# Kernel optimization log

Measured on AMD Instinct MI355X. Metric: run time of the kernel, lower is better.

The kernel has to match this reference:

```python
import jax, jax.numpy as jnp
import numpy as np

C = 256   # descriptor_dim
H = 4     # num_heads
D = C // H  # head_dim = 64
B, N = 8, 2048


def _conv1x1(x, w, b):
    # 1x1 Conv1d == per-position linear over channels: x [B,C,N], w [O,C], b [O]
    return jnp.einsum('oc,bcn->bon', w, x) + b[None, :, None]


def setup_inputs() -> dict:
    key = jax.random.key(0)
    ks = jax.random.split(key, 11)
    s = 1.0 / np.sqrt(C)
    return {
        'query': jax.random.normal(ks[0], (B, C, N), dtype=jnp.float32),
        'key':   jax.random.normal(ks[1], (B, C, N), dtype=jnp.float32),
        'value': jax.random.normal(ks[2], (B, C, N), dtype=jnp.float32),
        'wq': jax.random.normal(ks[3], (C, C), dtype=jnp.float32) * s,
        'bq': jax.random.normal(ks[4], (C,), dtype=jnp.float32) * s,
        'wk': jax.random.normal(ks[5], (C, C), dtype=jnp.float32) * s,
        'bk': jax.random.normal(ks[6], (C,), dtype=jnp.float32) * s,
        'wv': jax.random.normal(ks[7], (C, C), dtype=jnp.float32) * s,
        'bv': jax.random.normal(ks[8], (C,), dtype=jnp.float32) * s,
        'wm': jax.random.normal(ks[9], (C, C), dtype=jnp.float32) * s,
        'bm': jax.random.normal(ks[10], (C,), dtype=jnp.float32) * s,
    }


def reference(query, key, value, wq, bq, wk, bk, wv, bv, wm, bm):
    b = query.shape[0]
    # project then view channels as (head_dim, num_heads) -- matches torch .view order
    q = _conv1x1(query, wq, bq).reshape(b, D, H, -1)   # [B,D,H,N]
    k = _conv1x1(key,   wk, bk).reshape(b, D, H, -1)   # [B,D,H,M]
    v = _conv1x1(value, wv, bv).reshape(b, D, H, -1)   # [B,D,H,M]
    scores = jnp.einsum('bdhn,bdhm->bhnm', q, k) / (D ** 0.5)
    probs = jax.nn.softmax(scores, axis=-1)            # [B,H,N,M]
    out = jnp.einsum('bhnm,bdhm->bdhn', probs, v)      # [B,D,H,N]
    out = out.reshape(b, D * H, -1)                    # [B,C,N]
    return _conv1x1(out, wm, bm)
```

## Files before the change

kernel.cpp:

```cpp
#include <hip/hip_runtime.h>
#include <hip/hip_bf16.h>

typedef float f32x4 __attribute__((ext_vector_type(4)));
typedef float f32x16 __attribute__((ext_vector_type(16)));
typedef __bf16 bf16x8 __attribute__((ext_vector_type(8)));
typedef __bf16 bf16x4 __attribute__((ext_vector_type(4)));
typedef unsigned int uint2v __attribute__((ext_vector_type(2)));
typedef unsigned int u32;

constexpr int B_ = 8, C_ = 256, N_ = 2048, H_ = 4, D_ = 64;
constexpr int BH_ = B_ * H_;
constexpr size_t PER_ = (size_t)BH_ * N_ * D_;
constexpr float LOG2E = 1.44269504088896340736f;

static __device__ __forceinline__ float fast_exp2(float x) {
#if __has_builtin(__builtin_amdgcn_exp2f)
  return __builtin_amdgcn_exp2f(x);
#else
  return exp2f(x);
#endif
}

static __device__ __forceinline__ void* swz(void* base, int row, int cb) {
  return (char*)base + row * 128 + (cb ^ ((row & 7) << 4));
}
static __device__ __forceinline__ const void* swz(const void* base, int row, int cb) {
  return (const char*)base + row * 128 + (cb ^ ((row & 7) << 4));
}

static __device__ __forceinline__ void gload16(void* lds, const void* g) {
  __builtin_amdgcn_global_load_lds(
      (const __attribute__((address_space(1))) u32*)g,
      (__attribute__((address_space(3))) u32*)lds, 16, 0, 0);
}

struct W4 {
  const float* s0; const float* s1; const float* s2; const float* s3;
  __bf16* d0; __bf16* d1; __bf16* d2; __bf16* d3;
};

__global__ __launch_bounds__(256) void wcvt_kernel(W4 p) {
  const int m = blockIdx.y;
  const float* src = m == 0 ? p.s0 : m == 1 ? p.s1 : m == 2 ? p.s2 : p.s3;
  __bf16* dst = m == 0 ? p.d0 : m == 1 ? p.d1 : m == 2 ? p.d2 : p.d3;
  const int f = blockIdx.x * 256 + threadIdx.x;
  const int o_blk = f >> 9;
  const int ks = (f >> 6) & 7;
  const int lane = f & 63;
  const int row = o_blk * 16 + (lane & 15);
  const int kbase = ks * 32 + (lane >> 4) * 8;
  bf16x8 v;
  if (m == 3) {
    for (int e = 0; e < 8; e++) {
      const int k = kbase + e;
      const int c = ((k & 63) << 2) | (k >> 6);
      v[e] = (__bf16)src[row * 256 + c];
    }
  } else {
    const int srow = ((row & 63) << 2) | (row >> 6);
    const float* s = src + srow * 256 + kbase;
    float4 a = *(const float4*)s;
    float4 b = *(const float4*)(s + 4);
    v[0] = (__bf16)a.x; v[1] = (__bf16)a.y; v[2] = (__bf16)a.z; v[3] = (__bf16)a.w;
    v[4] = (__bf16)b.x; v[5] = (__bf16)b.y; v[6] = (__bf16)b.z; v[7] = (__bf16)b.w;
  }
  *(bf16x8*)&dst[(size_t)f * 8] = v;
}

__global__ __launch_bounds__(256) void qkv_fused_kernel(
    const float* __restrict__ xq, const float* __restrict__ xk,
    const float* __restrict__ xv, const __bf16* __restrict__ wfq,
    const __bf16* __restrict__ wfk, const __bf16* __restrict__ wfv,
    const float* __restrict__ bq, const float* __restrict__ bk,
    const float* __restrict__ bv, __bf16* __restrict__ oq,
    char* __restrict__ oksw, char* __restrict__ ovsw) {
  __shared__ __bf16 xlds[64][264];

  const int m = blockIdx.x >> 8;
  int inner = blockIdx.x & 255;
  inner = (inner & 7) * 32 + (inner >> 3);
  const int b = inner >> 5, nb = inner & 31;
  const int n0 = nb * 64;

  const float* xf = m == 0 ? xq : m == 1 ? xk : xv;
  const __bf16* wf = m == 0 ? wfq : m == 1 ? wfk : wfv;
  const float* bias = m == 0 ? bq : m == 1 ? bk : bv;
  const float scale = m == 0 ? 0.125f * LOG2E : 1.0f;

  const int t = threadIdx.x;
  {
    const int kl = t & 15;
    const int nl = (t >> 4) * 4;
    const float* src = xf + (size_t)b * C_ * N_ + n0 + nl;
    for (int kp = 0; kp < 8; kp++) {
      const int k = kp * 32 + kl * 2;
      float4 f0 = *(const float4*)(src + (size_t)k * N_);
      float4 f1 = *(const float4*)(src + (size_t)(k + 1) * N_);
      union { __bf16 h[2]; u32 u; } c0, c1, c2, c3;
      c0.h[0] = (__bf16)f0.x; c0.h[1] = (__bf16)f1.x;
      c1.h[0] = (__bf16)f0.y; c1.h[1] = (__bf16)f1.y;
      c2.h[0] = (__bf16)f0.z; c2.h[1] = (__bf16)f1.z;
      c3.h[0] = (__bf16)f0.w; c3.h[1] = (__bf16)f1.w;
      *(u32*)&xlds[nl + 0][k] = c0.u;
      *(u32*)&xlds[nl + 1][k] = c1.u;
      *(u32*)&xlds[nl + 2][k] = c2.u;
      *(u32*)&xlds[nl + 3][k] = c3.u;
    }
  }
  __syncthreads();

  const int lane = t & 63, wvv = t >> 6;
  const int wm = wvv >> 1, wn = wvv & 1;
  const int l15 = lane & 15, lg = lane >> 4;

  f32x4 acc[8][2] = {};

  for (int ks = 0; ks < 8; ks++) {
    bf16x8 bfr[2];
    for (int ni = 0; ni < 2; ni++)
      bfr[ni] = *(const bf16x8*)&xlds[wn * 32 + ni * 16 + l15][ks * 32 + lg * 8];
    for (int mi = 0; mi < 8; mi++) {
      bf16x8 af = *(const bf16x8*)&wf[(((size_t)(wm * 8 + mi) * 8 + ks) * 64 + lane) * 8];
      acc[mi][0] = __builtin_amdgcn_mfma_f32_16x16x32_bf16(af, bfr[0], acc[mi][0], 0, 0, 0);
      acc[mi][1] = __builtin_amdgcn_mfma_f32_16x16x32_bf16(af, bfr[1], acc[mi][1], 0, 0, 0);
    }
  }

  for (int mi = 0; mi < 8; mi++) {
    const int h = wm * 2 + (mi >> 2);
    const int d0 = (mi & 3) * 16 + 4 * lg;
    for (int ni = 0; ni < 2; ni++) {
      const int n = n0 + wn * 32 + ni * 16 + l15;
      const size_t tbase = ((size_t)(b * H_ + h) * (N_ / 64) + (n >> 6)) * 8192;
      if (m == 0) {
        bf16x4 o4;
        for (int r = 0; r < 4; r++)
          o4[r] = (__bf16)((acc[mi][ni][r] + bias[((d0 + r) << 2) | h]) * scale);
        *(bf16x4*)&oq[((size_t)(b * H_ + h) * N_ + n) * D_ + d0] = o4;
      } else if (m == 1) {
        bf16x4 o4;
        for (int r = 0; r < 4; r++)
          o4[r] = (__bf16)(acc[mi][ni][r] + bias[((d0 + r) << 2) | h]);
        *(bf16x4*)swz(oksw + tbase, n & 63, 2 * d0) = o4;
      } else {
        for (int r = 0; r < 4; r++)
          *(__bf16*)swz(ovsw + tbase, d0 + r, 2 * (n & 63)) =
              (__bf16)(acc[mi][ni][r] + bias[((d0 + r) << 2) | h]);
      }
    }
  }
}

template <int COMB>
__global__ __launch_bounds__(256) void final_proj_kernel(
    const __bf16* __restrict__ p0, const __bf16* __restrict__ p1,
    const float* __restrict__ l0, const float* __restrict__ l1,
    const __bf16* __restrict__ wf, const float* __restrict__ bias,
    float* __restrict__ out) {
  const int bid = blockIdx.x;
  const int wid = (bid & 7) * 128 + (bid >> 3);
  const int o_t = wid & 3;
  const int nb = (wid >> 2) & 31;
  const int b = wid >> 7;
  const int o0 = o_t * 64, n0 = nb * 64;
  const int t = threadIdx.x, lane = t & 63;
  const int wvv = t >> 6, wm = wvv >> 1, wn = wvv & 1;
  const int l15 = lane & 15, lg = lane >> 4;
  const int nbase = n0 + wn * 32 + l15;

  float inv[2][4];
  if constexpr (COMB) {
    for (int ni = 0; ni < 2; ni++)
      for (int h = 0; h < 4; h++) {
        const size_t bhn = (size_t)(b * H_ + h) * N_ + nbase + ni * 16;
        inv[ni][h] = 1.f / (l0[bhn] + l1[bhn]);
      }
  }

  f32x4 acc[2][2] = {};

  for (int ks = 0; ks < 8; ks++) {
    bf16x8 af[2];
    for (int mi = 0; mi < 2; mi++)
      af[mi] = *(const bf16x8*)&wf[(((size_t)(o_t * 4 + wm * 2 + mi) * 8 + ks) * 64 + lane) * 8];
    bf16x8 bfr[2];
    const int h = ks >> 1;
    const size_t bh = (size_t)(b * H_ + h);
    const int d0 = (ks & 1) * 32 + lg * 8;
    for (int ni = 0; ni < 2; ni++) {
      const size_t off = (bh * N_ + nbase + ni * 16) * D_ + d0;
      bf16x8 a = *(const bf16x8*)&p0[off];
      if constexpr (COMB) {
        bf16x8 bb = *(const bf16x8*)&p1[off];
        const float iv = inv[ni][h];
        bf16x8 r;
#pragma unroll
        for (int e = 0; e < 8; e++)
          r[e] = (__bf16)(((float)a[e] + (float)bb[e]) * iv);
        bfr[ni] = r;
      } else {
        bfr[ni] = a;
      }
    }
    for (int mi = 0; mi < 2; mi++)
      for (int ni = 0; ni < 2; ni++)
        acc[mi][ni] = __builtin_amdgcn_mfma_f32_16x16x32_bf16(
            af[mi], bfr[ni], acc[mi][ni], 0, 0, 0);
  }

  for (int mi = 0; mi < 2; mi++) {
    for (int r = 0; r < 4; r++) {
      const int och = o0 + wm * 32 + mi * 16 + 4 * lg + r;
      const float bv_ = bias[och];
      for (int ni = 0; ni < 2; ni++) {
        const int n = n0 + wn * 32 + ni * 16 + l15;
        out[((size_t)b * C_ + och) * N_ + n] = acc[mi][ni][r] + bv_;
      }
    }
  }
}

template <int SPLIT>
__global__ __launch_bounds__(256) void attn_kernel(
    const __bf16* __restrict__ qb, const char* __restrict__ kbsw,
    const char* __restrict__ vtsw, __bf16* __restrict__ pO,
    float* __restrict__ lbuf) {
  __shared__ char smem[32768];

  const int t = threadIdx.x, lane = t & 63, wv = t >> 6;
  const int l31 = lane & 31, hi = lane >> 5;

  const int bid = blockIdx.x;
  const int per_xcd = (512 * SPLIT) / 8;
  const int wid = (bid & 7) * per_xcd + (bid >> 3);
  const int bh = wid / (16 * SPLIT);
  const int rem = wid % (16 * SPLIT);
  const int qt = rem & 15;
  const int s = rem >> 4;
  const int qn = qt * 128 + wv * 32;
  constexpr int NT = N_ / SPLIT / 64;
  const int jt0 = s * NT;

  const char* ktiles = kbsw + (size_t)bh * (N_ / 64) * 8192;
  const char* vtiles = vtsw + (size_t)bh * (N_ / 64) * 8192;

  const __bf16* qrow = qb + ((size_t)bh * N_ + qn + l31) * D_;
  bf16x8 qf[4];
#pragma unroll
  for (int i = 0; i < 4; i++) qf[i] = *(const bf16x8*)(qrow + i * 16 + hi * 8);

  auto stage = [&](int jt_g, int bb) {
    const char* kt = ktiles + (size_t)jt_g * 8192;
    const char* vt = vtiles + (size_t)jt_g * 8192;
    gload16(smem + bb * 8192 + t * 16, kt + t * 16);
    gload16(smem + bb * 8192 + 4096 + t * 16, kt + 4096 + t * 16);
    gload16(smem + 16384 + bb * 8192 + t * 16, vt + t * 16);
    gload16(smem + 16384 + bb * 8192 + 4096 + t * 16, vt + 4096 + t * 16);
  };

  stage(jt0, 0);
  __syncthreads();

  f32x16 o0 = {}, o1 = {};
  float la0 = 0.f, la1 = 0.f, la2 = 0.f, la3 = 0.f;
  int cur = 0;

  for (int jt = 0; jt < NT; jt++) {
    if (jt + 1 < NT) stage(jt0 + jt + 1, cur ^ 1);
    const char* kc = smem + cur * 8192;
    const char* vc = smem + 16384 + cur * 8192;

    f32x16 s0 = {}, s1 = {};
    __builtin_amdgcn_s_setprio(1);
#pragma unroll
    for (int i = 0; i < 4; i++) {
      bf16x8 kf = *(const bf16x8*)swz(kc, l31, i * 32 + hi * 16);
      s0 = __builtin_amdgcn_mfma_f32_32x32x16_bf16(kf, qf[i], s0, 0, 0, 0);
    }
#pragma unroll
    for (int i = 0; i < 4; i++) {
      bf16x8 kf = *(const bf16x8*)swz(kc, 32 + l31, i * 32 + hi * 16);
      s1 = __builtin_amdgcn_mfma_f32_32x32x16_bf16(kf, qf[i], s1, 0, 0, 0);
    }
    __builtin_amdgcn_s_setprio(0);

#pragma unroll
    for (int sub = 0; sub < 2; sub++) {
      const f32x16 sv = sub ? s1 : s0;
      float pr[16];
#pragma unroll
      for (int r = 0; r < 16; r++) pr[r] = fast_exp2(sv[r]);
      la0 += pr[0] + pr[4] + pr[8] + pr[12];
      la1 += pr[1] + pr[5] + pr[9] + pr[13];
      la2 += pr[2] + pr[6] + pr[10] + pr[14];
      la3 += pr[3] + pr[7] + pr[11] + pr[15];
      unsigned w[8];
#pragma unroll
      for (int g = 0; g < 8; g++) {
        union { __bf16 h[2]; unsigned u; } cv;
        cv.h[0] = (__bf16)pr[2 * g];
        cv.h[1] = (__bf16)pr[2 * g + 1];
        w[g] = cv.u;
      }
      uint2v r0 = __builtin_amdgcn_permlane32_swap(w[0], w[2], false, false);
      uint2v r1 = __builtin_amdgcn_permlane32_swap(w[1], w[3], false, false);
      uint2v r2 = __builtin_amdgcn_permlane32_swap(w[4], w[6], false, false);
      uint2v r3 = __builtin_amdgcn_permlane32_swap(w[5], w[7], false, false);
      union { unsigned u[4]; bf16x8 v; } f0 = {{r0.x, r1.x, r0.y, r1.y}};
      union { unsigned u[4]; bf16x8 v; } f1 = {{r2.x, r3.x, r2.y, r3.y}};
      const int scb = sub * 64;
      __builtin_amdgcn_s_setprio(1);
      {
        bf16x8 vf = *(const bf16x8*)swz(vc, l31, scb + hi * 16);
        o0 = __builtin_amdgcn_mfma_f32_32x32x16_bf16(vf, f0.v, o0, 0, 0, 0);
        vf = *(const bf16x8*)swz(vc, l31, scb + 32 + hi * 16);
        o0 = __builtin_amdgcn_mfma_f32_32x32x16_bf16(vf, f1.v, o0, 0, 0, 0);
        vf = *(const bf16x8*)swz(vc, 32 + l31, scb + hi * 16);
        o1 = __builtin_amdgcn_mfma_f32_32x32x16_bf16(vf, f0.v, o1, 0, 0, 0);
        vf = *(const bf16x8*)swz(vc, 32 + l31, scb + 32 + hi * 16);
        o1 = __builtin_amdgcn_mfma_f32_32x32x16_bf16(vf, f1.v, o1, 0, 0, 0);
      }
      __builtin_amdgcn_s_setprio(0);
    }

    __syncthreads();
    cur ^= 1;
  }

  float la = la0 + la1 + la2 + la3;
  la += __shfl_xor(la, 32);
  const float scl = (SPLIT == 1) ? 1.f / la : 1.f;

  if constexpr (SPLIT > 1) {
    if (hi == 0)
      lbuf[(size_t)s * BH_ * N_ + (size_t)bh * N_ + qn + l31] = la;
  }

  char* ep = smem + wv * 4096;
#pragma unroll
  for (int dt = 0; dt < 2; dt++) {
    const f32x16 o = dt ? o1 : o0;
#pragma unroll
    for (int g = 0; g < 4; g++) {
      bf16x4 o4;
#pragma unroll
      for (int j = 0; j < 4; j++) o4[j] = (__bf16)(o[4 * g + j] * scl);
      *(bf16x4*)swz(ep, l31, dt * 64 + 16 * g + 8 * hi) = o4;
    }
  }
  asm volatile("" ::: "memory");
  {
    __bf16* dst = pO + (size_t)s * PER_ + ((size_t)bh * N_ + qn) * D_;
#pragma unroll
    for (int i = 0; i < 4; i++) {
      const int row = i * 8 + (lane >> 3);
      uint4 v = *(const uint4*)swz(ep, row, (lane & 7) * 16);
      *(uint4*)((char*)dst + i * 1024 + lane * 16) = v;
    }
  }
}

extern "C" void kernel_launch(void* const* d_in, const int* in_sizes, int n_in,
                              void* d_out, int out_size, void* d_ws,
                              size_t ws_size, hipStream_t stream) {
  const float* query = (const float*)d_in[0];
  const float* key_ = (const float*)d_in[1];
  const float* value = (const float*)d_in[2];
  const float* wq = (const float*)d_in[3];
  const float* bq = (const float*)d_in[4];
  const float* wk = (const float*)d_in[5];
  const float* bk = (const float*)d_in[6];
  const float* wv = (const float*)d_in[7];
  const float* bv = (const float*)d_in[8];
  const float* wm = (const float*)d_in[9];
  const float* bm = (const float*)d_in[10];

  __bf16* qb = (__bf16*)d_ws;
  char* kbsw = (char*)(qb + PER_);
  char* vtsw = kbsw + PER_ * 2;
  __bf16* p0 = (__bf16*)(vtsw + PER_ * 2);
  __bf16* p1 = p0 + PER_;
  float* lbuf = (float*)(p1 + PER_);
  __bf16* wfq = (__bf16*)(lbuf + 2 * BH_ * N_);
  __bf16* wfk = wfq + 65536;
  __bf16* wfv = wfk + 65536;
  __bf16* wfm = wfv + 65536;

  const size_t need_split = (size_t)((char*)(wfm + 65536) - (char*)d_ws);
  const bool use_split = ws_size >= need_split;

  dim3 blk(256);
  W4 wp{wq, wk, wv, wm, wfq, wfk, wfv, wfm};
  if (!use_split) {
    wfq = p1; wfk = wfq + 65536; wfv = wfk + 65536; wfm = wfv + 65536;
    wp = W4{wq, wk, wv, wm, wfq, wfk, wfv, wfm};
  }
  wcvt_kernel<<<dim3(32, 4), blk, 0, stream>>>(wp);

  qkv_fused_kernel<<<768, blk, 0, stream>>>(query, key_, value, wfq, wfk, wfv,
                                            bq, bk, bv, qb, kbsw, vtsw);
  if (use_split) {
    attn_kernel<2><<<1024, blk, 0, stream>>>(qb, kbsw, vtsw, p0, lbuf);
    final_proj_kernel<1><<<1024, blk, 0, stream>>>(
        p0, p1, lbuf, lbuf + BH_ * N_, wfm, bm, (float*)d_out);
  } else {
    attn_kernel<1><<<512, blk, 0, stream>>>(qb, kbsw, vtsw, p0, nullptr);
    final_proj_kernel<0><<<1024, blk, 0, stream>>>(
        p0, p0, nullptr, nullptr, wfm, bm, (float*)d_out);
  }
}
```

Before: 106.5 us.

## Use 512-thread attention blocks with 4-way KV split and generalized combine

The attention kernel now runs 8 waves per block, covering 256 query rows that share each staged K/V tile, so each thread loads half as much per tile. The key dimension is split up to 4 ways when workspace allows, which restores the block count. The final projection is generalized to sum NS partial outputs and NS row-sum buffers before normalizing. This raises K/V reuse per block and keeps parallelism, but the combine step reads more partial data and needs more workspace. The workspace layout is reordered to fit the extra partials.

```diff
diff --git a/kernel.cpp b/kernel.cpp
--- a/kernel.cpp
+++ b/kernel.cpp
@@ -151,10 +151,9 @@
   }
 }
 
-template <int COMB>
+template <int NS>
 __global__ __launch_bounds__(256) void final_proj_kernel(
-    const __bf16* __restrict__ p0, const __bf16* __restrict__ p1,
-    const float* __restrict__ l0, const float* __restrict__ l1,
+    const __bf16* __restrict__ p, const float* __restrict__ lb,
     const __bf16* __restrict__ wf, const float* __restrict__ bias,
     float* __restrict__ out) {
   const int bid = blockIdx.x;
@@ -169,11 +168,14 @@
   const int nbase = n0 + wn * 32 + l15;
 
   float inv[2][4];
-  if constexpr (COMB) {
+  if constexpr (NS > 1) {
     for (int ni = 0; ni < 2; ni++)
       for (int h = 0; h < 4; h++) {
         const size_t bhn = (size_t)(b * H_ + h) * N_ + nbase + ni * 16;
-        inv[ni][h] = 1.f / (l0[bhn] + l1[bhn]);
+        float ls = 0.f;
+#pragma unroll
+        for (int u = 0; u < NS; u++) ls += lb[(size_t)u * BH_ * N_ + bhn];
+        inv[ni][h] = 1.f / ls;
       }
   }
 
@@ -189,17 +191,21 @@
     const int d0 = (ks & 1) * 32 + lg * 8;
     for (int ni = 0; ni < 2; ni++) {
       const size_t off = (bh * N_ + nbase + ni * 16) * D_ + d0;
-      bf16x8 a = *(const bf16x8*)&p0[off];
-      if constexpr (COMB) {
-        bf16x8 bb = *(const bf16x8*)&p1[off];
+      if constexpr (NS == 1) {
+        bfr[ni] = *(const bf16x8*)&p[off];
+      } else {
+        float s8[8] = {};
+#pragma unroll
+        for (int u = 0; u < NS; u++) {
+          bf16x8 a = *(const bf16x8*)&p[(size_t)u * PER_ + off];
+#pragma unroll
+          for (int e = 0; e < 8; e++) s8[e] += (float)a[e];
+        }
         const float iv = inv[ni][h];
         bf16x8 r;
 #pragma unroll
-        for (int e = 0; e < 8; e++)
-          r[e] = (__bf16)(((float)a[e] + (float)bb[e]) * iv);
+        for (int e = 0; e < 8; e++) r[e] = (__bf16)(s8[e] * iv);
         bfr[ni] = r;
-      } else {
-        bfr[ni] = a;
       }
     }
     for (int mi = 0; mi < 2; mi++)
@@ -221,7 +227,7 @@
 }
 
 template <int SPLIT>
-__global__ __launch_bounds__(256) void attn_kernel(
+__global__ __launch_bounds__(512) void attn_kernel(
     const __bf16* __restrict__ qb, const char* __restrict__ kbsw,
     const char* __restrict__ vtsw, __bf16* __restrict__ pO,
     float* __restrict__ lbuf) {
@@ -231,13 +237,13 @@
   const int l31 = lane & 31, hi = lane >> 5;
 
   const int bid = blockIdx.x;
-  const int per_xcd = (512 * SPLIT) / 8;
+  const int per_xcd = (256 * SPLIT) / 8;
   const int wid = (bid & 7) * per_xcd + (bid >> 3);
-  const int bh = wid / (16 * SPLIT);
-  const int rem = wid % (16 * SPLIT);
-  const int qt = rem & 15;
-  const int s = rem >> 4;
-  const int qn = qt * 128 + wv * 32;
+  const int bh = wid / (8 * SPLIT);
+  const int rem = wid % (8 * SPLIT);
+  const int qt = rem % 8;
+  const int s = rem / 8;
+  const int qn = qt * 256 + wv * 32;
   constexpr int NT = N_ / SPLIT / 64;
   const int jt0 = s * NT;
 
@@ -250,12 +256,9 @@
   for (int i = 0; i < 4; i++) qf[i] = *(const bf16x8*)(qrow + i * 16 + hi * 8);
 
   auto stage = [&](int jt_g, int bb) {
-    const char* kt = ktiles + (size_t)jt_g * 8192;
-    const char* vt = vtiles + (size_t)jt_g * 8192;
-    gload16(smem + bb * 8192 + t * 16, kt + t * 16);
-    gload16(smem + bb * 8192 + 4096 + t * 16, kt + 4096 + t * 16);
-    gload16(smem + 16384 + bb * 8192 + t * 16, vt + t * 16);
-    gload16(smem + 16384 + bb * 8192 + 4096 + t * 16, vt + 4096 + t * 16);
+    gload16(smem + bb * 8192 + t * 16, ktiles + (size_t)jt_g * 8192 + t * 16);
+    gload16(smem + 16384 + bb * 8192 + t * 16,
+            vtiles + (size_t)jt_g * 8192 + t * 16);
   };
 
   stage(jt0, 0);
@@ -378,34 +381,34 @@
   __bf16* qb = (__bf16*)d_ws;
   char* kbsw = (char*)(qb + PER_);
   char* vtsw = kbsw + PER_ * 2;
-  __bf16* p0 = (__bf16*)(vtsw + PER_ * 2);
-  __bf16* p1 = p0 + PER_;
-  float* lbuf = (float*)(p1 + PER_);
-  __bf16* wfq = (__bf16*)(lbuf + 2 * BH_ * N_);
+  float* lbuf = (float*)(vtsw + PER_ * 2);
+  __bf16* wfq = (__bf16*)(lbuf + 4 * BH_ * N_);
   __bf16* wfk = wfq + 65536;
   __bf16* wfv = wfk + 65536;
   __bf16* wfm = wfv + 65536;
-
-  const size_t need_split = (size_t)((char*)(wfm + 65536) - (char*)d_ws);
-  const bool use_split = ws_size >= need_split;
+  __bf16* p0 = wfm + 65536;
+
+  const size_t fixed = (size_t)((char*)p0 - (char*)d_ws);
+  const int ns = (ws_size >= fixed + 4 * PER_ * 2) ? 4
+               : (ws_size >= fixed + 2 * PER_ * 2) ? 2 : 1;
 
   dim3 blk(256);
   W4 wp{wq, wk, wv, wm, wfq, wfk, wfv, wfm};
-  if (!use_split) {
-    wfq = p1; wfk = wfq + 65536; wfv = wfk + 65536; wfm = wfv + 65536;
-    wp = W4{wq, wk, wv, wm, wfq, wfk, wfv, wfm};
-  }
   wcvt_kernel<<<dim3(32, 4), blk, 0, stream>>>(wp);
 
   qkv_fused_kernel<<<768, blk, 0, stream>>>(query, key_, value, wfq, wfk, wfv,
                                             bq, bk, bv, qb, kbsw, vtsw);
-  if (use_split) {
-    attn_kernel<2><<<1024, blk, 0, stream>>>(qb, kbsw, vtsw, p0, lbuf);
-    final_proj_kernel<1><<<1024, blk, 0, stream>>>(
-        p0, p1, lbuf, lbuf + BH_ * N_, wfm, bm, (float*)d_out);
+  if (ns == 4) {
+    attn_kernel<4><<<1024, dim3(512), 0, stream>>>(qb, kbsw, vtsw, p0, lbuf);
+    final_proj_kernel<4><<<1024, blk, 0, stream>>>(p0, lbuf, wfm, bm,
+                                                   (float*)d_out);
+  } else if (ns == 2) {
+    attn_kernel<2><<<512, dim3(512), 0, stream>>>(qb, kbsw, vtsw, p0, lbuf);
+    final_proj_kernel<2><<<1024, blk, 0, stream>>>(p0, lbuf, wfm, bm,
+                                                   (float*)d_out);
   } else {
-    attn_kernel<1><<<512, blk, 0, stream>>>(qb, kbsw, vtsw, p0, nullptr);
-    final_proj_kernel<0><<<1024, blk, 0, stream>>>(
-        p0, p0, nullptr, nullptr, wfm, bm, (float*)d_out);
-  }
-}
+    attn_kernel<1><<<256, dim3(512), 0, stream>>>(qb, kbsw, vtsw, p0, nullptr);
+    final_proj_kernel<1><<<1024, blk, 0, stream>>>(p0, nullptr, wfm, bm,
+                                                   (float*)d_out);
+  }
+}
```

New measurement: 117.8 us. +10.6%, slower.
